# Optimization experiments

Measured on AMD Instinct MI355X. Metric: run time of the kernel, lower is better.

## Reference

```python
import jax, jax.numpy as jnp
import numpy as np

NUM_HEADS = 16

def setup_inputs() -> dict:
    key = jax.random.key(0)
    ks = jax.random.split(key, 5)
    B, T, C = 2, 2048, 1024
    s = 0.02
    return {
        "x": jax.random.normal(ks[0], (B, T, C), dtype=jnp.float32),
        "attn_w": jax.random.normal(ks[1], (3 * C, C), dtype=jnp.float32) * s,
        "attn_b": jax.random.normal(ks[2], (3 * C,), dtype=jnp.float32) * s,
        "proj_w": jax.random.normal(ks[3], (C, C), dtype=jnp.float32) * s,
        "proj_b": jax.random.normal(ks[4], (C,), dtype=jnp.float32) * s,
    }

def reference(x, attn_w, attn_b, proj_w, proj_b):
    B, T, C = x.shape
    H = NUM_HEADS
    D = C // H
    # fused QKV projection (torch Linear: x @ W^T + b)
    qkv = x @ attn_w.T + attn_b                      # [B, T, 3C]
    q, k, v = jnp.split(qkv, 3, axis=-1)             # each [B, T, C]
    # split heads -> [B, H, T, D]
    def heads(t):
        return t.reshape(B, T, H, D).transpose(0, 2, 1, 3)
    q, k, v = heads(q), heads(k), heads(v)
    scale = 1.0 / jnp.sqrt(jnp.asarray(D, dtype=x.dtype))
    scores = jnp.einsum("bhtd,bhsd->bhts", q, k) * scale   # [B, H, T, T]
    causal = jnp.tril(jnp.ones((T, T), dtype=bool))
    scores = jnp.where(causal[None, None], scores, jnp.asarray(-jnp.inf, dtype=scores.dtype))
    att = jax.nn.softmax(scores, axis=-1)
    out = jnp.einsum("bhts,bhsd->bhtd", att, v)      # [B, H, T, D]
    out = out.transpose(0, 2, 1, 3).reshape(B, T, C)
    return out @ proj_w.T + proj_b
```

## Files before the change

kernel.cpp:

```cpp
#include <hip/hip_runtime.h>
#include <hip/hip_bf16.h>

typedef __bf16 bf16_t;
typedef __bf16 bf16x4 __attribute__((ext_vector_type(4)));
typedef __bf16 bf16x8 __attribute__((ext_vector_type(8)));
typedef float f32x4 __attribute__((ext_vector_type(4)));
typedef float f32x8 __attribute__((ext_vector_type(8)));

#define MFMA16(a, b, c) __builtin_amdgcn_mfma_f32_16x16x32_bf16(a, b, c, 0, 0, 0)

#define GLOAD_LDS16(g, l)                                              \
  __builtin_amdgcn_global_load_lds(                                    \
      (const __attribute__((address_space(1))) unsigned int*)(g),      \
      (__attribute__((address_space(3))) unsigned int*)(l), 16, 0, 0)

constexpr int B = 2, T = 2048, C = 1024, H = 16, D = 64;
constexpr int NQKV = 3 * C;
constexpr int M = B * T;

__global__ __launch_bounds__(256) void cvt_kernel(
    const float* __restrict__ s0, bf16_t* __restrict__ d0, int n0,
    const float* __restrict__ s1, bf16_t* __restrict__ d1, int n1,
    const float* __restrict__ s2, bf16_t* __restrict__ d2, int n2)
{
  const float* s; bf16_t* d; int n;
  if (blockIdx.y == 0)      { s = s0; d = d0; n = n0; }
  else if (blockIdx.y == 1) { s = s1; d = d1; n = n1; }
  else                      { s = s2; d = d2; n = n2; }
  const int idx = (blockIdx.x * 256 + threadIdx.x) * 8;
  if (idx >= n) return;
  f32x8 t = *(const f32x8*)(s + idx);
  bf16x8 r;
#pragma unroll
  for (int j = 0; j < 8; ++j) r[j] = (bf16_t)t[j];
  *(bf16x8*)(d + idx) = r;
}

template<int BN, int NI>
__device__ __forceinline__ void gemm_mainloop_db(
    const bf16_t* __restrict__ A, const bf16_t* __restrict__ Wt,
    const int K, const int m0, const int n0,
    bf16_t* ldsA0, bf16_t* ldsA1, bf16_t* ldsB0, bf16_t* ldsB1,
    f32x4 acc[4][NI])
{
  const int tid  = threadIdx.x;
  const int wv   = tid >> 6;
  const int lane = tid & 63;
  const int col  = lane & 15;
  const int quad = lane >> 4;
  const int lr8  = lane >> 3;
  const int cpos = lane & 7;
  const int wm = wv >> 1, wn = wv & 1;
  constexpr int BJ = BN / 32;
  constexpr int BRW = BN / 4;

  const bf16_t* ag[4]; const bf16_t* bg[BJ];
#pragma unroll
  for (int j = 0; j < 4; ++j)
    ag[j] = A + (size_t)(m0 + wv * 32 + j * 8 + lr8) * K + (cpos ^ lr8) * 8;
#pragma unroll
  for (int j = 0; j < BJ; ++j)
    bg[j] = Wt + (size_t)(n0 + wv * BRW + j * 8 + lr8) * K + (cpos ^ lr8) * 8;

  const int xa = quad ^ (col & 7);
  const int niter = K / 64;

#pragma unroll
  for (int j = 0; j < 4; ++j)
    GLOAD_LDS16(ag[j], ldsA0 + (wv * 32 + j * 8) * 64);
#pragma unroll
  for (int j = 0; j < BJ; ++j)
    GLOAD_LDS16(bg[j], ldsB0 + (wv * BRW + j * 8) * 64);

  for (int it = 0; it < niter; ++it) {
    __syncthreads();
    const bf16_t* cA = (it & 1) ? ldsA1 : ldsA0;
    const bf16_t* cB = (it & 1) ? ldsB1 : ldsB0;
    if (it + 1 < niter) {
      bf16_t* nA = (it & 1) ? ldsA0 : ldsA1;
      bf16_t* nB = (it & 1) ? ldsB0 : ldsB1;
      const int off = (it + 1) * 64;
#pragma unroll
      for (int j = 0; j < 4; ++j)
        GLOAD_LDS16(ag[j] + off, nA + (wv * 32 + j * 8) * 64);
#pragma unroll
      for (int j = 0; j < BJ; ++j)
        GLOAD_LDS16(bg[j] + off, nB + (wv * BRW + j * 8) * 64);
    }
#pragma unroll
    for (int ks = 0; ks < 2; ++ks) {
      const int xk = (xa ^ (ks * 4)) * 8;
      bf16x8 af[4], bfr[NI];
#pragma unroll
      for (int mi = 0; mi < 4; ++mi)
        af[mi] = *(const bf16x8*)(cA + (wm * 64 + mi * 16 + col) * 64 + xk);
#pragma unroll
      for (int ni = 0; ni < NI; ++ni)
        bfr[ni] = *(const bf16x8*)(cB + (wn * (NI * 16) + ni * 16 + col) * 64 + xk);
#pragma unroll
      for (int mi = 0; mi < 4; ++mi)
#pragma unroll
        for (int ni = 0; ni < NI; ++ni)
          acc[mi][ni] = MFMA16(af[mi], bfr[ni], acc[mi][ni]);
    }
  }
}

__global__ __launch_bounds__(256) void qkv_gemm_kernel(
    const bf16_t* __restrict__ x, const bf16_t* __restrict__ w,
    const float* __restrict__ bias,
    bf16_t* __restrict__ qws, bf16_t* __restrict__ kws, bf16_t* __restrict__ vws)
{
  __shared__ __align__(16) bf16_t ldsA[2][128 * 64];
  __shared__ __align__(16) bf16_t ldsB[2][128 * 64];
  const int lane = threadIdx.x & 63;
  const int wv   = threadIdx.x >> 6;
  const int col  = lane & 15;
  const int quad = lane >> 4;
  const int wm = wv >> 1, wn = wv & 1;
  const int m0 = blockIdx.y * 128;
  const int n0 = blockIdx.x * 128;

  f32x4 acc[4][4] = {};
  gemm_mainloop_db<128, 4>(x, w, C, m0, n0,
                           ldsA[0], ldsA[1], ldsB[0], ldsB[1], acc);

  const int which = n0 >> 10;

  if (which == 2) {
    __syncthreads();
    bf16_t* vt = &ldsA[0][0] + wv * 4096;

#pragma unroll
    for (int ni = 0; ni < 4; ++ni) {
      const int n = n0 + wn * 64 + ni * 16 + col;
      const float bval = bias[n];
      const int d = n & 63;
#pragma unroll
      for (int r = 0; r < 4; ++r) {
        bf16x4 pw;
#pragma unroll
        for (int mi = 0; mi < 4; ++mi)
          pw[mi] = (bf16_t)(acc[mi][ni][r] + bval);
        const int k = 2 * quad + (r >> 1);
        const int S = d * 8 + (k ^ (d & 7));
        *(bf16x4*)(vt + S * 8 + (r & 1) * 4) = pw;
      }
    }

    const int b   = (m0 + wm * 64) >> 11;
    const int t0w = (m0 + wm * 64) & (T - 1);
    const int h   = ((n0 & (C - 1)) + wn * 64) >> 6;
    const size_t bh = (size_t)(b * H + h);
    const int lr8 = lane >> 3;
    const int c8  = lane & 7;
#pragma unroll
    for (int j = 0; j < 8; ++j) {
      const int d = j * 8 + lr8;
      bf16x8 row = *(const bf16x8*)(vt + (d * 8 + (c8 ^ (d & 7))) * 8);
      *(bf16x8*)(vws + (bh * D + d) * T + t0w + c8 * 8) = row;
    }
  } else {
#pragma unroll
    for (int ni = 0; ni < 4; ++ni) {
      const int n = n0 + wn * 64 + ni * 16 + col;
      const float bval = bias[n];
      const int c = n & (C - 1);
      const int h = c >> 6;
      const int d = c & 63;
#pragma unroll
      for (int mi = 0; mi < 4; ++mi) {
#pragma unroll
        for (int r = 0; r < 4; ++r) {
          const int m = m0 + wm * 64 + mi * 16 + quad * 4 + r;
          const int b = m >> 11;
          const int t = m & (T - 1);
          const bf16_t bv = (bf16_t)(acc[mi][ni][r] + bval);
          const size_t bh = (size_t)(b * H + h);
          if (which == 0) qws[(bh * T + t) * D + d] = bv;
          else            kws[(bh * T + t) * D + d] = bv;
        }
      }
    }
  }
}

__global__ __launch_bounds__(256) void attn_kernel(
    const bf16_t* __restrict__ qws, const bf16_t* __restrict__ kws,
    const bf16_t* __restrict__ vws, bf16_t* __restrict__ yws)
{
  const int id = blockIdx.x;
  const int bh = id & 31;
  const int pr = id >> 5;
  const int tid  = threadIdx.x;
  const int wv   = tid >> 6;
  const int lane = tid & 63;
  const int col  = lane & 15;
  const int quad = lane >> 4;

  const bf16_t* Q  = qws + (size_t)bh * T * D;
  const bf16_t* K  = kws + (size_t)bh * T * D;
  const bf16_t* Vt = vws + (size_t)bh * D * T;

  __shared__ __align__(16) bf16_t ldsK[2][64 * 64];
  __shared__ __align__(16) bf16_t ldsV[2][64 * 64];
  __shared__ __align__(16) bf16_t ldsP[4][16 * 64];
  bf16_t* ldsPw = ldsP[wv];

  const float cscale = 0.125f * 1.44269504088896340736f;

  const int xs   = col & 7;
  const int cxq  = (quad ^ xs) * 8;
  const int lr8  = lane >> 3;
  const int ksrc = (lane & 7) ^ lr8;
  const int pxor = (quad & 1) * 4;
  const int b = bh >> 4;
  const int h = bh & 15;

  const int qt_h = 31 - pr, qt_l = pr;
  const int t0h = qt_h * 64, t0l = qt_l * 64;
  const int twh = t0h + 16 * wv, twl = t0l + 16 * wv;
  const int niter = qt_h + 1;

  bf16x8 qfh0 = *(const bf16x8*)(Q + (size_t)(twh + col) * D + quad * 8);
  bf16x8 qfh1 = *(const bf16x8*)(Q + (size_t)(twh + col) * D + 32 + quad * 8);
  bf16x8 qfl0 = *(const bf16x8*)(Q + (size_t)(twl + col) * D + quad * 8);
  bf16x8 qfl1 = *(const bf16x8*)(Q + (size_t)(twl + col) * D + 32 + quad * 8);

  f32x4 oh[4] = {}, ol[4] = {};
  f32x4 lph = {}, lpl = {};

  auto compute_tile = [&](const bf16_t* bK, const bf16_t* bV, int s0, int tw,
                          int t0, bf16x8 qf0, bf16x8 qf1,
                          f32x4 (&o)[4], f32x4& lp) {
    f32x4 sc[4];
#pragma unroll
    for (int kb = 0; kb < 4; ++kb) {
      const bf16_t* kr = bK + (kb * 16 + col) * 64;
      bf16x8 kf0 = *(const bf16x8*)(kr + cxq);
      bf16x8 kf1 = *(const bf16x8*)(kr + (cxq ^ 32));
      f32x4 a = {};
      a = MFMA16(qf0, kf0, a);
      a = MFMA16(qf1, kf1, a);
      sc[kb] = a;
    }
    const bool diag = (s0 == t0);
#pragma unroll
    for (int r = 0; r < 4; ++r) {
      const int prow = (quad * 4 + r) * 64;
      const int pxr  = pxor + r;
      bf16x4 pw;
#pragma unroll
      for (int kb = 0; kb < 4; ++kb) {
        float p = __builtin_amdgcn_exp2f(sc[kb][r] * cscale);
        if (diag && (s0 + kb * 16 + col > tw + quad * 4 + r)) p = 0.0f;
        lp[r] += p;
        pw[kb] = (bf16_t)p;
      }
      *(bf16x4*)(ldsPw + prow + (((col >> 1) ^ pxr) * 8) + (col & 1) * 4) = pw;
    }
#pragma unroll
    for (int ks = 0; ks < 2; ++ks) {
      const int xk = cxq ^ (ks * 32);
      bf16x8 pa = *(const bf16x8*)(ldsPw + col * 64 + xk);
#pragma unroll
      for (int ni = 0; ni < 4; ++ni) {
        bf16x8 vf = *(const bf16x8*)(bV + (ni * 16 + col) * 64 + xk);
        o[ni] = MFMA16(pa, vf, o[ni]);
      }
    }
  };

#pragma unroll
  for (int j = 0; j < 2; ++j) {
    GLOAD_LDS16(K + (size_t)(16 * wv + j * 8 + lr8) * D + ksrc * 8,
                ldsK[0] + (16 * wv + j * 8) * 64);
    GLOAD_LDS16(Vt + (size_t)(16 * wv + j * 8 + lr8) * T + ksrc * 8,
                ldsV[0] + (16 * wv + j * 8) * 64);
  }

  for (int it = 0; it < niter; ++it) {
    const int s0 = it * 64;
    __syncthreads();

    if (it + 1 < niter) {
      const int sn = s0 + 64;
      bf16_t* dK = ldsK[(it + 1) & 1];
      bf16_t* dV = ldsV[(it + 1) & 1];
#pragma unroll
      for (int j = 0; j < 2; ++j) {
        GLOAD_LDS16(K + (size_t)(sn + 16 * wv + j * 8 + lr8) * D + ksrc * 8,
                    dK + (16 * wv + j * 8) * 64);
        GLOAD_LDS16(Vt + (size_t)(16 * wv + j * 8 + lr8) * T + sn + ksrc * 8,
                    dV + (16 * wv + j * 8) * 64);
      }
    }

    const bf16_t* bK = ldsK[it & 1];
    const bf16_t* bV = ldsV[it & 1];

    compute_tile(bK, bV, s0, twh, t0h, qfh0, qfh1, oh, lph);
    if (s0 <= t0l)
      compute_tile(bK, bV, s0, twl, t0l, qfl0, qfl1, ol, lpl);
  }

#pragma unroll
  for (int r = 0; r < 4; ++r) {
    float l0 = lph[r], l1 = lpl[r];
#pragma unroll
    for (int off = 1; off < 16; off <<= 1) {
      l0 += __shfl_xor(l0, off);
      l1 += __shfl_xor(l1, off);
    }
    const float rl0 = 1.0f / l0, rl1 = 1.0f / l1;
    const int th = twh + quad * 4 + r;
    const int tl = twl + quad * 4 + r;
#pragma unroll
    for (int ni = 0; ni < 4; ++ni) {
      const int d = ni * 16 + col;
      yws[((size_t)(b * T + th)) * C + h * D + d] = (bf16_t)(oh[ni][r] * rl0);
      yws[((size_t)(b * T + tl)) * C + h * D + d] = (bf16_t)(ol[ni][r] * rl1);
    }
  }
}

__global__ __launch_bounds__(256) void proj_gemm_kernel(
    const bf16_t* __restrict__ y, const bf16_t* __restrict__ w,
    const float* __restrict__ bias, float* __restrict__ out)
{
  __shared__ __align__(16) bf16_t ldsA[2][128 * 64];
  __shared__ __align__(16) bf16_t ldsB[2][64 * 64];
  const int lane = threadIdx.x & 63;
  const int wv   = threadIdx.x >> 6;
  const int col  = lane & 15;
  const int quad = lane >> 4;
  const int wm = wv >> 1, wn = wv & 1;
  const int m0 = blockIdx.y * 128;
  const int n0 = blockIdx.x * 64;

  f32x4 acc[4][2] = {};
  gemm_mainloop_db<64, 2>(y, w, C, m0, n0,
                          ldsA[0], ldsA[1], ldsB[0], ldsB[1], acc);

#pragma unroll
  for (int ni = 0; ni < 2; ++ni) {
    const int n = n0 + wn * 32 + ni * 16 + col;
    const float bval = bias[n];
#pragma unroll
    for (int mi = 0; mi < 4; ++mi) {
#pragma unroll
      for (int r = 0; r < 4; ++r) {
        const int m = m0 + wm * 64 + mi * 16 + quad * 4 + r;
        out[(size_t)m * C + n] = acc[mi][ni][r] + bval;
      }
    }
  }
}

extern "C" void kernel_launch(void* const* d_in, const int* in_sizes, int n_in,
                              void* d_out, int out_size, void* d_ws, size_t ws_size,
                              hipStream_t stream) {
  const float* x      = (const float*)d_in[0];
  const float* attn_w = (const float*)d_in[1];
  const float* attn_b = (const float*)d_in[2];
  const float* proj_w = (const float*)d_in[3];
  const float* proj_b = (const float*)d_in[4];
  float* out = (float*)d_out;

  const size_t E = (size_t)B * H * T * D;
  char* ws = (char*)d_ws;
  bf16_t* qws = (bf16_t*)(ws);
  bf16_t* kws = (bf16_t*)(ws + 2 * E);
  bf16_t* vws = (bf16_t*)(ws + 4 * E);
  bf16_t* yws = (bf16_t*)(ws + 6 * E);
  bf16_t* xb  = (bf16_t*)(ws + 8 * E);
  bf16_t* awb = (bf16_t*)(ws + 10 * E);
  bf16_t* pwb = (bf16_t*)(ws + 11 * E + E / 2);

  const int NX = M * C, NAW = NQKV * C, NPW = C * C;
  cvt_kernel<<<dim3(NX / 2048, 3), 256, 0, stream>>>(
      x, xb, NX, attn_w, awb, NAW, proj_w, pwb, NPW);
  qkv_gemm_kernel<<<dim3(NQKV / 128, M / 128), 256, 0, stream>>>(
      xb, awb, attn_b, qws, kws, vws);
  attn_kernel<<<512, 256, 0, stream>>>(qws, kws, vws, yws);
  proj_gemm_kernel<<<dim3(C / 64, M / 128), 256, 0, stream>>>(
      yws, pwb, proj_b, out);
}
```

Baseline: 169.2 us.

## Fold softmax scale into Q and interleave high/low query tiles sharing K/V fragments

Multiplies Q by 0.125*log2(e) in the QKV epilogue, so the attention loop applies exp2 directly without a per-score multiply. Fuses the two per-iteration tile computations so each K and V fragment read from LDS feeds both the high and low query tiles. This doubles the P scratch buffer and interleaves the independent MFMA chains. It also sets launch_bounds min-blocks to 2, which may add register pressure from keeping both score sets live, and rounding Q to bf16 after scaling changes numerics slightly.

```diff
diff --git a/kernel.cpp b/kernel.cpp
--- a/kernel.cpp
+++ b/kernel.cpp
@@ -17,6 +17,8 @@
 constexpr int B = 2, T = 2048, C = 1024, H = 16, D = 64;
 constexpr int NQKV = 3 * C;
 constexpr int M = B * T;
+
+#define QSCALE 0.18033688011112042f
 
 __global__ __launch_bounds__(256) void cvt_kernel(
     const float* __restrict__ s0, bf16_t* __restrict__ d0, int n0,
@@ -175,17 +177,18 @@
           const int m = m0 + wm * 64 + mi * 16 + quad * 4 + r;
           const int b = m >> 11;
           const int t = m & (T - 1);
-          const bf16_t bv = (bf16_t)(acc[mi][ni][r] + bval);
           const size_t bh = (size_t)(b * H + h);
-          if (which == 0) qws[(bh * T + t) * D + d] = bv;
-          else            kws[(bh * T + t) * D + d] = bv;
+          if (which == 0)
+            qws[(bh * T + t) * D + d] = (bf16_t)((acc[mi][ni][r] + bval) * QSCALE);
+          else
+            kws[(bh * T + t) * D + d] = (bf16_t)(acc[mi][ni][r] + bval);
         }
       }
     }
   }
 }
 
-__global__ __launch_bounds__(256) void attn_kernel(
+__global__ __launch_bounds__(256, 2) void attn_kernel(
     const bf16_t* __restrict__ qws, const bf16_t* __restrict__ kws,
     const bf16_t* __restrict__ vws, bf16_t* __restrict__ yws)
 {
@@ -204,10 +207,9 @@
 
   __shared__ __align__(16) bf16_t ldsK[2][64 * 64];
   __shared__ __align__(16) bf16_t ldsV[2][64 * 64];
-  __shared__ __align__(16) bf16_t ldsP[4][16 * 64];
-  bf16_t* ldsPw = ldsP[wv];
-
-  const float cscale = 0.125f * 1.44269504088896340736f;
+  __shared__ __align__(16) bf16_t ldsP[8][16 * 64];
+  bf16_t* ldsPh = ldsP[wv * 2];
+  bf16_t* ldsPl = ldsP[wv * 2 + 1];
 
   const int xs   = col & 7;
   const int cxq  = (quad ^ xs) * 8;
@@ -230,78 +232,108 @@
   f32x4 oh[4] = {}, ol[4] = {};
   f32x4 lph = {}, lpl = {};
 
-  auto compute_tile = [&](const bf16_t* bK, const bf16_t* bV, int s0, int tw,
-                          int t0, bf16x8 qf0, bf16x8 qf1,
-                          f32x4 (&o)[4], f32x4& lp) {
-    f32x4 sc[4];
+#pragma unroll
+  for (int j = 0; j < 2; ++j) {
+    GLOAD_LDS16(K + (size_t)(16 * wv + j * 8 + lr8) * D + ksrc * 8,
+                ldsK[0] + (16 * wv + j * 8) * 64);
+    GLOAD_LDS16(Vt + (size_t)(16 * wv + j * 8 + lr8) * T + ksrc * 8,
+                ldsV[0] + (16 * wv + j * 8) * 64);
+  }
+
+  for (int it = 0; it < niter; ++it) {
+    const int s0 = it * 64;
+    __syncthreads();
+
+    if (it + 1 < niter) {
+      const int sn = s0 + 64;
+      bf16_t* dK = ldsK[(it + 1) & 1];
+      bf16_t* dV = ldsV[(it + 1) & 1];
+#pragma unroll
+      for (int j = 0; j < 2; ++j) {
+        GLOAD_LDS16(K + (size_t)(sn + 16 * wv + j * 8 + lr8) * D + ksrc * 8,
+                    dK + (16 * wv + j * 8) * 64);
+        GLOAD_LDS16(Vt + (size_t)(16 * wv + j * 8 + lr8) * T + sn + ksrc * 8,
+                    dV + (16 * wv + j * 8) * 64);
+      }
+    }
+
+    const bf16_t* bK = ldsK[it & 1];
+    const bf16_t* bV = ldsV[it & 1];
+    const bool dual = (s0 <= t0l);
+
+    f32x4 sch[4], scl[4];
 #pragma unroll
     for (int kb = 0; kb < 4; ++kb) {
       const bf16_t* kr = bK + (kb * 16 + col) * 64;
       bf16x8 kf0 = *(const bf16x8*)(kr + cxq);
       bf16x8 kf1 = *(const bf16x8*)(kr + (cxq ^ 32));
       f32x4 a = {};
-      a = MFMA16(qf0, kf0, a);
-      a = MFMA16(qf1, kf1, a);
-      sc[kb] = a;
-    }
-    const bool diag = (s0 == t0);
-#pragma unroll
-    for (int r = 0; r < 4; ++r) {
-      const int prow = (quad * 4 + r) * 64;
-      const int pxr  = pxor + r;
-      bf16x4 pw;
-#pragma unroll
-      for (int kb = 0; kb < 4; ++kb) {
-        float p = __builtin_amdgcn_exp2f(sc[kb][r] * cscale);
-        if (diag && (s0 + kb * 16 + col > tw + quad * 4 + r)) p = 0.0f;
-        lp[r] += p;
-        pw[kb] = (bf16_t)p;
-      }
-      *(bf16x4*)(ldsPw + prow + (((col >> 1) ^ pxr) * 8) + (col & 1) * 4) = pw;
-    }
+      a = MFMA16(qfh0, kf0, a);
+      a = MFMA16(qfh1, kf1, a);
+      sch[kb] = a;
+      if (dual) {
+        f32x4 al = {};
+        al = MFMA16(qfl0, kf0, al);
+        al = MFMA16(qfl1, kf1, al);
+        scl[kb] = al;
+      }
+    }
+
+    {
+      const bool diag = (s0 == t0h);
+#pragma unroll
+      for (int r = 0; r < 4; ++r) {
+        const int prow = (quad * 4 + r) * 64;
+        const int pxr  = pxor + r;
+        bf16x4 pw;
+#pragma unroll
+        for (int kb = 0; kb < 4; ++kb) {
+          float p = __builtin_amdgcn_exp2f(sch[kb][r]);
+          if (diag && (s0 + kb * 16 + col > twh + quad * 4 + r)) p = 0.0f;
+          lph[r] += p;
+          pw[kb] = (bf16_t)p;
+        }
+        *(bf16x4*)(ldsPh + prow + (((col >> 1) ^ pxr) * 8) + (col & 1) * 4) = pw;
+      }
+    }
+    if (dual) {
+      const bool diag = (s0 == t0l);
+#pragma unroll
+      for (int r = 0; r < 4; ++r) {
+        const int prow = (quad * 4 + r) * 64;
+        const int pxr  = pxor + r;
+        bf16x4 pw;
+#pragma unroll
+        for (int kb = 0; kb < 4; ++kb) {
+          float p = __builtin_amdgcn_exp2f(scl[kb][r]);
+          if (diag && (s0 + kb * 16 + col > twl + quad * 4 + r)) p = 0.0f;
+          lpl[r] += p;
+          pw[kb] = (bf16_t)p;
+        }
+        *(bf16x4*)(ldsPl + prow + (((col >> 1) ^ pxr) * 8) + (col & 1) * 4) = pw;
+      }
+    }
+
 #pragma unroll
     for (int ks = 0; ks < 2; ++ks) {
       const int xk = cxq ^ (ks * 32);
-      bf16x8 pa = *(const bf16x8*)(ldsPw + col * 64 + xk);
-#pragma unroll
-      for (int ni = 0; ni < 4; ++ni) {
-        bf16x8 vf = *(const bf16x8*)(bV + (ni * 16 + col) * 64 + xk);
-        o[ni] = MFMA16(pa, vf, o[ni]);
-      }
-    }
-  };
-
-#pragma unroll
-  for (int j = 0; j < 2; ++j) {
-    GLOAD_LDS16(K + (size_t)(16 * wv + j * 8 + lr8) * D + ksrc * 8,
-                ldsK[0] + (16 * wv + j * 8) * 64);
-    GLOAD_LDS16(Vt + (size_t)(16 * wv + j * 8 + lr8) * T + ksrc * 8,
-                ldsV[0] + (16 * wv + j * 8) * 64);
-  }
-
-  for (int it = 0; it < niter; ++it) {
-    const int s0 = it * 64;
-    __syncthreads();
-
-    if (it + 1 < niter) {
-      const int sn = s0 + 64;
-      bf16_t* dK = ldsK[(it + 1) & 1];
-      bf16_t* dV = ldsV[(it + 1) & 1];
-#pragma unroll
-      for (int j = 0; j < 2; ++j) {
-        GLOAD_LDS16(K + (size_t)(sn + 16 * wv + j * 8 + lr8) * D + ksrc * 8,
-                    dK + (16 * wv + j * 8) * 64);
-        GLOAD_LDS16(Vt + (size_t)(16 * wv + j * 8 + lr8) * T + sn + ksrc * 8,
-                    dV + (16 * wv + j * 8) * 64);
-      }
-    }
-
-    const bf16_t* bK = ldsK[it & 1];
-    const bf16_t* bV = ldsV[it & 1];
-
-    compute_tile(bK, bV, s0, twh, t0h, qfh0, qfh1, oh, lph);
-    if (s0 <= t0l)
-      compute_tile(bK, bV, s0, twl, t0l, qfl0, qfl1, ol, lpl);
+      bf16x8 pah = *(const bf16x8*)(ldsPh + col * 64 + xk);
+      if (dual) {
+        bf16x8 pal = *(const bf16x8*)(ldsPl + col * 64 + xk);
+#pragma unroll
+        for (int ni = 0; ni < 4; ++ni) {
+          bf16x8 vf = *(const bf16x8*)(bV + (ni * 16 + col) * 64 + xk);
+          oh[ni] = MFMA16(pah, vf, oh[ni]);
+          ol[ni] = MFMA16(pal, vf, ol[ni]);
+        }
+      } else {
+#pragma unroll
+        for (int ni = 0; ni < 4; ++ni) {
+          bf16x8 vf = *(const bf16x8*)(bV + (ni * 16 + col) * 64 + xk);
+          oh[ni] = MFMA16(pah, vf, oh[ni]);
+        }
+      }
+    }
   }
 
 #pragma unroll
```

New measurement: 175.6 us. 1.04x slower.
